# Performance work log

Measured on AMD Instinct MI355X. Metric: run time of the kernel, lower is better.

Reference implementation:

```python
import jax, jax.numpy as jnp
import numpy as np

V = 50000
D = 128
EF = 16
E = 800000
LN_EPS = 1e-5


def setup_inputs() -> dict:
    key = jax.random.key(0)
    ks = jax.random.split(key, 9)
    h = jax.random.normal(ks[0], (V, D), dtype=jnp.float32)
    edge_index = jax.random.randint(ks[1], (2, E), 0, V, dtype=jnp.int64)
    edge_attr = jax.random.normal(ks[2], (E, EF), dtype=jnp.float32)
    # msg_mlp = Linear(D+EF, D) -> ReLU -> Dropout(0) -> Linear(D, D)
    s1 = 1.0 / np.sqrt(D + EF)
    s2 = 1.0 / np.sqrt(D)
    W1 = jax.random.uniform(ks[3], (D + EF, D), minval=-s1, maxval=s1, dtype=jnp.float32)
    b1 = jax.random.uniform(ks[4], (D,), minval=-s1, maxval=s1, dtype=jnp.float32)
    W2 = jax.random.uniform(ks[5], (D, D), minval=-s2, maxval=s2, dtype=jnp.float32)
    b2 = jax.random.uniform(ks[6], (D,), minval=-s2, maxval=s2, dtype=jnp.float32)
    gamma = jnp.ones((D,), dtype=jnp.float32)
    beta = jnp.zeros((D,), dtype=jnp.float32)
    return {"h": h, "edge_index": edge_index, "edge_attr": edge_attr,
            "W1": W1, "b1": b1, "W2": W2, "b2": b2,
            "gamma": gamma, "beta": beta}


def _layer_norm(x, gamma, beta):
    mu = jnp.mean(x, axis=-1, keepdims=True)
    var = jnp.mean(jnp.square(x - mu), axis=-1, keepdims=True)
    return (x - mu) * jax.lax.rsqrt(var + LN_EPS) * gamma + beta


def reference(h, edge_index, edge_attr, W1, b1, W2, b2, gamma, beta):
    src, dst = edge_index[0], edge_index[1]
    # gather source node features, concat edge features: [E, D+EF]
    x = jnp.concatenate([h[src], edge_attr], axis=-1)
    # per-edge message MLP (dropout p=0 -> identity)
    msg = jax.nn.relu(x @ W1 + b1) @ W2 + b2  # [E, D]
    # scatter-add messages to destinations
    agg = jax.ops.segment_sum(msg, dst, num_segments=V)  # [V, D]
    # count initialized to ones BEFORE scatter_add -> denominator = 1 + in_degree
    deg = jax.ops.segment_sum(jnp.ones((E,), dtype=h.dtype), dst, num_segments=V)
    count = (1.0 + deg)[:, None]  # [V, 1]
    return _layer_norm(h + agg / count, gamma, beta)
```

## Files before the change

### kernel.cpp

```cpp
#include <hip/hip_runtime.h>
#include <hip/hip_bf16.h>

#define V 50000
#define D 128
#define EF 16
#define E_EDGES 800000
#define NT 12500
#define USTR 136
#define XESTR 40
#define CSTR 136
#define NSCAN 196
#define EGRID 1024
#define UGRID 782

typedef __attribute__((ext_vector_type(8))) __bf16 bf16x8;
typedef __attribute__((ext_vector_type(4))) float f32x4;
typedef __attribute__((ext_vector_type(2))) __fp16 fp16x2;

__device__ inline unsigned short f2bf(float f) {
    unsigned u = __float_as_uint(f);
    u += 0x7FFF + ((u >> 16) & 1);
    return (unsigned short)(u >> 16);
}
__device__ inline unsigned pack2(float a, float b) {
    return (unsigned)f2bf(a) | ((unsigned)f2bf(b) << 16);
}
__device__ inline float bf2f(unsigned short u) {
    return __uint_as_float((unsigned)u << 16);
}
__device__ inline unsigned pkbf(float a, float b) {
    union { __hip_bfloat162 h; unsigned u; } v;
    v.h = __float22bfloat162_rn(make_float2(a, b));
    return v.u;
}
__device__ inline unsigned pkf16(float a, float b) {
    union { fp16x2 h; unsigned u; } v;
    v.h = __builtin_amdgcn_cvt_pkrtz(a, b);
    return v.u;
}

__global__ __launch_bounds__(256)
void setup_kernel(const float* __restrict__ h, const int* __restrict__ ei,
                  int* __restrict__ cnt, float* __restrict__ agg,
                  const float* __restrict__ W1, const float* __restrict__ W2,
                  unsigned short* __restrict__ W1p, unsigned short* __restrict__ W2p,
                  unsigned short* __restrict__ U) {
    __shared__ __align__(16) unsigned short Hs[64 * USTR];
    const int tid = threadIdx.x;
    int idx = blockIdx.x * 256 + tid;
    *(float4*)(agg + ((size_t)idx << 2)) = (float4){0.f, 0.f, 0.f, 0.f};
    if (idx < E_EDGES) atomicAdd(&cnt[ei[E_EDGES + idx]], 1);
    if (idx < 5 * 128 * 32) {
        int kb = idx >> 12, rem = idx & 4095;
        int n = rem >> 5, kk = rem & 31;
        int k = kb * 32 + kk;
        W1p[idx] = f2bf((k < D + EF) ? W1[k * D + n] : 0.0f);
    }
    if (idx < 4 * 128 * 32) {
        int kb = idx >> 12, rem = idx & 4095;
        int n = rem >> 5, kk = rem & 31;
        W2p[idx] = f2bf(W2[(kb * 32 + kk) * D + n]);
    }
    if (blockIdx.x >= UGRID) return;

    const int lane = tid & 63;
    const int wave = tid >> 6;
    const int nlo  = lane & 15;
    const int kq   = lane >> 4;
    const int er   = tid >> 4;
    const int ec   = tid & 15;
    const int gbase = blockIdx.x << 6;

    bf16x8 B1[4][2];
    #pragma unroll
    for (int t = 0; t < 2; ++t) {
        int n = wave * 32 + t * 16 + nlo;
        #pragma unroll
        for (int kb = 0; kb < 4; ++kb) {
            union { bf16x8 v; unsigned short s[8]; } f;
            #pragma unroll
            for (int j = 0; j < 8; ++j)
                f.s[j] = f2bf(W1[(kb * 32 + (kq << 3) + j) * D + n]);
            B1[kb][t] = f.v;
        }
    }

    #pragma unroll
    for (int m = 0; m < 4; ++m) {
        int row = er + m * 16;
        int grow = gbase + row;
        unsigned* o = (unsigned*)(Hs + row * USTR + (ec << 3));
        if (grow < V) {
            const float4* p = (const float4*)(h + (size_t)grow * D + (ec << 3));
            float4 v0 = p[0], v1 = p[1];
            o[0] = pack2(v0.x, v0.y); o[1] = pack2(v0.z, v0.w);
            o[2] = pack2(v1.x, v1.y); o[3] = pack2(v1.z, v1.w);
        } else {
            o[0] = 0u; o[1] = 0u; o[2] = 0u; o[3] = 0u;
        }
    }
    __syncthreads();

    f32x4 acc[4][2];
    #pragma unroll
    for (int mt = 0; mt < 4; ++mt)
        #pragma unroll
        for (int t = 0; t < 2; ++t)
            acc[mt][t] = (f32x4){0.f, 0.f, 0.f, 0.f};

    #pragma unroll
    for (int kb = 0; kb < 4; ++kb) {
        bf16x8 A[4];
        int ko = kb * 32 + (kq << 3);
        #pragma unroll
        for (int mt = 0; mt < 4; ++mt)
            A[mt] = *(const bf16x8*)(Hs + (mt * 16 + nlo) * USTR + ko);
        #pragma unroll
        for (int mt = 0; mt < 4; ++mt)
            #pragma unroll
            for (int t = 0; t < 2; ++t)
                acc[mt][t] = __builtin_amdgcn_mfma_f32_16x16x32_bf16(A[mt], B1[kb][t], acc[mt][t], 0, 0, 0);
    }

    #pragma unroll
    for (int mt = 0; mt < 4; ++mt)
        #pragma unroll
        for (int t = 0; t < 2; ++t)
            #pragma unroll
            for (int r = 0; r < 4; ++r) {
                int row = mt * 16 + (kq << 2) + r;
                int grow = gbase + row;
                int col = wave * 32 + t * 16 + nlo;
                if (grow < V)
                    U[(size_t)grow * D + col] = f2bf(acc[mt][t][r]);
            }
}

__device__ inline int block_excl_scan(int x, int t, int* ws) {
    int lane = t & 63, w = t >> 6;
    int inc = x;
    #pragma unroll
    for (int off = 1; off < 64; off <<= 1) {
        int y = __shfl_up(inc, off);
        if (lane >= off) inc += y;
    }
    if (lane == 63) ws[w] = inc;
    __syncthreads();
    if (t == 0) {
        int r = 0;
        #pragma unroll
        for (int i = 0; i < 4; ++i) { int c = ws[i]; ws[i] = r; r += c; }
    }
    __syncthreads();
    return inc - x + ws[w];
}

__global__ __launch_bounds__(256)
void scan1_kernel(const int* __restrict__ cnt, int* __restrict__ cursor,
                  int* __restrict__ bsum) {
    __shared__ int ws[4];
    __shared__ int tot;
    int t = threadIdx.x;
    int i = blockIdx.x * 256 + t;
    int x = (i < V) ? cnt[i] : 0;
    int ex = block_excl_scan(x, t, ws);
    if (i < V) cursor[i] = ex;
    if (t == 255) tot = ex + x;
    __syncthreads();
    if (t == 0) bsum[blockIdx.x] = tot;
}

__global__ __launch_bounds__(256)
void scatter_kernel(const int* __restrict__ ei, int* __restrict__ cursor,
                    const int* __restrict__ bsum,
                    int* __restrict__ srcs, int* __restrict__ dsts,
                    int* __restrict__ eidx) {
    __shared__ int ws[4];
    __shared__ int sboff[NSCAN];
    int t = threadIdx.x;
    int x = (t < NSCAN) ? bsum[t] : 0;
    int ex = block_excl_scan(x, t, ws);
    if (t < NSCAN) sboff[t] = ex;
    __syncthreads();
    int e = blockIdx.x * 256 + t;
    int d = ei[E_EDGES + e];
    int pos = atomicAdd(&cursor[d], 1) + sboff[d >> 8];
    srcs[pos] = ei[e];
    dsts[pos] = d;
    eidx[pos] = e;
}

__global__ __launch_bounds__(256, 4)
void edge_kernel(const unsigned short* __restrict__ U,
                 const float* __restrict__ ea,
                 const int* __restrict__ srcs, const int* __restrict__ dsts,
                 const int* __restrict__ eidx,
                 const unsigned short* __restrict__ W1p, const unsigned short* __restrict__ W2p,
                 const float* __restrict__ b1, const float* __restrict__ b2,
                 float* __restrict__ agg) {
    __shared__ __align__(16) unsigned short Us[64 * USTR];
    __shared__ __align__(16) _Float16 Cs[64 * CSTR];
    __shared__ __align__(16) unsigned short Xe[64 * XESTR];
    __shared__ int sDst[2][64];

    const int tid  = threadIdx.x;
    const int lane = tid & 63;
    const int wave = tid >> 6;
    const int nlo  = lane & 15;
    const int kq   = lane >> 4;
    const int er   = tid >> 4;
    const int ec   = tid & 15;
    const int ee   = tid >> 2;
    const int eq   = tid & 3;

    bf16x8 B1e[2], B2[4][2];
    float4 b1n[2], b2n[2];
    #pragma unroll
    for (int t = 0; t < 2; ++t) {
        int n = wave * 32 + t * 16 + nlo;
        b1n[t] = *(const float4*)(b1 + wave * 32 + t * 16 + (kq << 2));
        b2n[t] = *(const float4*)(b2 + wave * 32 + t * 16 + (kq << 2));
        B1e[t] = *(const bf16x8*)(W1p + ((4 << 7) + n) * 32 + (kq << 3));
        #pragma unroll
        for (int kb = 0; kb < 4; ++kb)
            B2[kb][t] = *(const bf16x8*)(W2p + ((kb << 7) + n) * 32 + (kq << 3));
    }

    {
        unsigned* xz = (unsigned*)Xe;
        int i0 = tid, i1 = tid + 256;
        xz[(i0 >> 3) * (XESTR / 2) + 8 + (i0 & 7)] = 0u;
        xz[(i1 >> 3) * (XESTR / 2) + 8 + (i1 & 7)] = 0u;
    }

    const int base0 = blockIdx.x << 6;
    int a0 = srcs[base0 + er];
    int a1 = srcs[base0 + er + 16];
    int a2 = srcs[base0 + er + 32];
    int a3 = srcs[base0 + er + 48];
    int aev = eidx[base0 + ee];
    int ddcur = dsts[base0 + lane];
    bf16x8 pf0 = *(const bf16x8*)(U + (size_t)a0 * D + (ec << 3));
    bf16x8 pf1 = *(const bf16x8*)(U + (size_t)a1 * D + (ec << 3));
    bf16x8 pf2 = *(const bf16x8*)(U + (size_t)a2 * D + (ec << 3));
    bf16x8 pf3 = *(const bf16x8*)(U + (size_t)a3 * D + (ec << 3));
    float4 pfe = *(const float4*)(ea + (size_t)aev * EF + (eq << 2));

    int n1 = blockIdx.x + EGRID;
    int nb1 = (n1 < NT ? n1 : blockIdx.x) << 6;
    int i1s0 = srcs[nb1 + er];
    int i1s1 = srcs[nb1 + er + 16];
    int i1s2 = srcs[nb1 + er + 32];
    int i1s3 = srcs[nb1 + er + 48];
    int i1e  = eidx[nb1 + ee];
    int i1d  = dsts[nb1 + lane];

    int buf = 0;
    for (int tile = blockIdx.x; tile < NT; tile += EGRID) {
        if (tid < 64) sDst[buf][tid] = ddcur;
        *(bf16x8*)(Us + er * USTR + (ec << 3))        = pf0;
        *(bf16x8*)(Us + (er + 16) * USTR + (ec << 3)) = pf1;
        *(bf16x8*)(Us + (er + 32) * USTR + (ec << 3)) = pf2;
        *(bf16x8*)(Us + (er + 48) * USTR + (ec << 3)) = pf3;
        {
            unsigned* xp = (unsigned*)Xe + ee * (XESTR / 2) + (eq << 1);
            xp[0] = pkbf(pfe.x, pfe.y);
            xp[1] = pkbf(pfe.z, pfe.w);
        }
        __syncthreads();

        f32x4 accE[4][2];
        #pragma unroll
        for (int mt = 0; mt < 4; ++mt)
            #pragma unroll
            for (int t = 0; t < 2; ++t) {
                uint2 uu = *(const uint2*)(Us + (mt * 16 + nlo) * USTR + wave * 32 + t * 16 + (kq << 2));
                accE[mt][t][0] = bf2f((unsigned short)uu.x);
                accE[mt][t][1] = bf2f((unsigned short)(uu.x >> 16));
                accE[mt][t][2] = bf2f((unsigned short)uu.y);
                accE[mt][t][3] = bf2f((unsigned short)(uu.y >> 16));
            }
        {
            bf16x8 Xf[4];
            #pragma unroll
            for (int mt = 0; mt < 4; ++mt)
                Xf[mt] = *(const bf16x8*)(Xe + (mt * 16 + nlo) * XESTR + (kq << 3));
            #pragma unroll
            for (int mt = 0; mt < 4; ++mt)
                #pragma unroll
                for (int t = 0; t < 2; ++t)
                    accE[mt][t] = __builtin_amdgcn_mfma_f32_16x16x32_bf16(B1e[t], Xf[mt], accE[mt][t], 0, 0, 0);
        }

        #pragma unroll
        for (int mt = 0; mt < 4; ++mt)
            #pragma unroll
            for (int t = 0; t < 2; ++t) {
                uint2 yw;
                yw.x = pkbf(fmaxf(accE[mt][t][0] + b1n[t].x, 0.0f),
                            fmaxf(accE[mt][t][1] + b1n[t].y, 0.0f));
                yw.y = pkbf(fmaxf(accE[mt][t][2] + b1n[t].z, 0.0f),
                            fmaxf(accE[mt][t][3] + b1n[t].w, 0.0f));
                *(uint2*)(Us + (mt * 16 + nlo) * USTR + wave * 32 + t * 16 + (kq << 2)) = yw;
            }
        __syncthreads();

        f32x4 acc2[4][2];
        #pragma unroll
        for (int mt = 0; mt < 4; ++mt)
            #pragma unroll
            for (int t = 0; t < 2; ++t)
                acc2[mt][t] = (f32x4){0.f, 0.f, 0.f, 0.f};

        #pragma unroll
        for (int kb = 0; kb < 4; ++kb) {
            bf16x8 Yf[4];
            int ko = kb * 32 + (kq << 3);
            #pragma unroll
            for (int mt = 0; mt < 4; ++mt)
                Yf[mt] = *(const bf16x8*)(Us + (mt * 16 + nlo) * USTR + ko);
            #pragma unroll
            for (int mt = 0; mt < 4; ++mt)
                #pragma unroll
                for (int t = 0; t < 2; ++t)
                    acc2[mt][t] = __builtin_amdgcn_mfma_f32_16x16x32_bf16(B2[kb][t], Yf[mt], acc2[mt][t], 0, 0, 0);
        }

        #pragma unroll
        for (int mt = 0; mt < 4; ++mt)
            #pragma unroll
            for (int t = 0; t < 2; ++t) {
                uint2 cw;
                cw.x = pkf16(acc2[mt][t][0] + b2n[t].x, acc2[mt][t][1] + b2n[t].y);
                cw.y = pkf16(acc2[mt][t][2] + b2n[t].z, acc2[mt][t][3] + b2n[t].w);
                *(uint2*)((unsigned short*)Cs + (size_t)(mt * 16 + nlo) * CSTR + wave * 32 + t * 16 + (kq << 2)) = cw;
            }
        __syncthreads();

        int n2 = tile + 2 * EGRID;
        int nb2 = (n2 < NT ? n2 : tile) << 6;
        int i2s0 = srcs[nb2 + er];
        int i2s1 = srcs[nb2 + er + 16];
        int i2s2 = srcs[nb2 + er + 32];
        int i2s3 = srcs[nb2 + er + 48];
        int i2e  = eidx[nb2 + ee];
        int i2d  = dsts[nb2 + lane];

        bf16x8 q0 = *(const bf16x8*)(U + (size_t)i1s0 * D + (ec << 3));
        bf16x8 q1 = *(const bf16x8*)(U + (size_t)i1s1 * D + (ec << 3));
        bf16x8 q2 = *(const bf16x8*)(U + (size_t)i1s2 * D + (ec << 3));
        bf16x8 q3 = *(const bf16x8*)(U + (size_t)i1s3 * D + (ec << 3));
        float4 qe = *(const float4*)(ea + (size_t)i1e * EF + (eq << 2));
        int nextdd = i1d;

        {
            int col = tid & 127;
            int rbase = (tid >> 7) << 5;
            float sum = 0.f;
            int cur = sDst[buf][rbase];
            for (int i = 0; i < 32; ++i) {
                int d = sDst[buf][rbase + i];
                if (d != cur) {
                    atomicAdd(&agg[(size_t)cur * D + col], sum);
                    sum = 0.f;
                    cur = d;
                }
                sum += (float)Cs[(rbase + i) * CSTR + col];
            }
            atomicAdd(&agg[(size_t)cur * D + col], sum);
        }

        pf0 = q0; pf1 = q1; pf2 = q2; pf3 = q3; pfe = qe; ddcur = nextdd;
        i1s0 = i2s0; i1s1 = i2s1; i1s2 = i2s2; i1s3 = i2s3; i1e = i2e; i1d = i2d;
        buf ^= 1;
    }
}

__global__ __launch_bounds__(256)
void finalize_kernel(const float* __restrict__ h, const float* __restrict__ agg,
                     const int* __restrict__ cnt,
                     const float* __restrict__ gamma, const float* __restrict__ beta,
                     float* __restrict__ out) {
    int wave = threadIdx.x >> 6, lane = threadIdx.x & 63;
    int v = blockIdx.x * 4 + wave;
    if (v >= V) return;
    float inv = 1.0f / (1.0f + (float)cnt[v]);
    const float* hr = h + (size_t)v * D;
    const float* ar = agg + (size_t)v * D;
    float x0 = hr[lane]      + ar[lane]      * inv;
    float x1 = hr[lane + 64] + ar[lane + 64] * inv;
    float s = x0 + x1;
    #pragma unroll
    for (int m = 32; m; m >>= 1) s += __shfl_xor(s, m);
    float mu = s * (1.0f / 128.0f);
    float d0 = x0 - mu, d1 = x1 - mu;
    float vs = d0 * d0 + d1 * d1;
    #pragma unroll
    for (int m = 32; m; m >>= 1) vs += __shfl_xor(vs, m);
    float rs = rsqrtf(vs * (1.0f / 128.0f) + 1e-5f);
    out[(size_t)v * D + lane]      = d0 * rs * gamma[lane]      + beta[lane];
    out[(size_t)v * D + 64 + lane] = d1 * rs * gamma[lane + 64] + beta[lane + 64];
}

extern "C" void kernel_launch(void* const* d_in, const int* in_sizes, int n_in,
                              void* d_out, int out_size, void* d_ws, size_t ws_size,
                              hipStream_t stream) {
    const float* h     = (const float*)d_in[0];
    const int*   ei    = (const int*)d_in[1];
    const float* ea    = (const float*)d_in[2];
    const float* W1    = (const float*)d_in[3];
    const float* b1    = (const float*)d_in[4];
    const float* W2    = (const float*)d_in[5];
    const float* b2    = (const float*)d_in[6];
    const float* gamma = (const float*)d_in[7];
    const float* beta  = (const float*)d_in[8];
    float* out = (float*)d_out;

    char* ws = (char*)d_ws;
    float*          agg    = (float*)ws;
    int*            cnt    = (int*)(ws + 25600000);
    int*            cursor = (int*)(ws + 25800000);
    int*            bsum   = (int*)(ws + 26000000);
    int*            srcs   = (int*)(ws + 26000800);
    int*            dsts   = (int*)(ws + 29200800);
    int*            eidx   = (int*)(ws + 32400800);
    unsigned short* W1p    = (unsigned short*)(ws + 35600800);
    unsigned short* W2p    = (unsigned short*)(ws + 35641760);
    unsigned short* U      = (unsigned short*)(ws + 35674528);

    (void)hipMemsetAsync(cnt, 0, 200000, stream);
    setup_kernel<<<6250, 256, 0, stream>>>(h, ei, cnt, agg, W1, W2, W1p, W2p, U);
    scan1_kernel<<<NSCAN, 256, 0, stream>>>(cnt, cursor, bsum);
    scatter_kernel<<<3125, 256, 0, stream>>>(ei, cursor, bsum, srcs, dsts, eidx);
    edge_kernel<<<EGRID, 256, 0, stream>>>(U, ea, srcs, dsts, eidx, W1p, W2p, b1, b2, agg);
    finalize_kernel<<<12500, 256, 0, stream>>>(h, agg, cnt, gamma, beta, out);
}
```

Measured before the change: 302.5 us.

## Double edge tile to 128 rows with shared Us/Cs LDS union

Grows the per-block edge tile from 64 to 128 edges, so each wave reuses its register-resident W1/W2 fragments across twice as many MFMA rows and the segmented scatter runs over longer sorted runs, which means fewer atomics. The Us and Cs LDS buffers are overlaid in a union to hold shared memory down. This adds extra barriers, removes the double-buffered sDst, and lowers the occupancy hint from 4 to 3 blocks per CU with a grid of 768. Register pressure rises from 8 prefetched gather vectors and 16 accumulators, which risks spills or lower occupancy.

```diff
diff --git a/kernel.cpp b/kernel.cpp
--- a/kernel.cpp
+++ b/kernel.cpp
@@ -5,12 +5,11 @@
 #define D 128
 #define EF 16
 #define E_EDGES 800000
-#define NT 12500
+#define NIT 6250
 #define USTR 136
 #define XESTR 40
-#define CSTR 136
 #define NSCAN 196
-#define EGRID 1024
+#define EGRID 768
 #define UGRID 782
 
 typedef __attribute__((ext_vector_type(8))) __bf16 bf16x8;
@@ -190,7 +189,7 @@
     eidx[pos] = e;
 }
 
-__global__ __launch_bounds__(256, 4)
+__global__ __launch_bounds__(256, 3)
 void edge_kernel(const unsigned short* __restrict__ U,
                  const float* __restrict__ ea,
                  const int* __restrict__ srcs, const int* __restrict__ dsts,
@@ -198,10 +197,13 @@
                  const unsigned short* __restrict__ W1p, const unsigned short* __restrict__ W2p,
                  const float* __restrict__ b1, const float* __restrict__ b2,
                  float* __restrict__ agg) {
-    __shared__ __align__(16) unsigned short Us[64 * USTR];
-    __shared__ __align__(16) _Float16 Cs[64 * CSTR];
-    __shared__ __align__(16) unsigned short Xe[64 * XESTR];
-    __shared__ int sDst[2][64];
+    union SU {
+        unsigned short Us[128 * USTR];
+        _Float16 Cs[128 * USTR];
+    };
+    __shared__ __align__(16) SU u;
+    __shared__ __align__(16) unsigned short Xe[128 * XESTR];
+    __shared__ int sDst[128];
 
     const int tid  = threadIdx.x;
     const int lane = tid & 63;
@@ -210,8 +212,8 @@
     const int kq   = lane >> 4;
     const int er   = tid >> 4;
     const int ec   = tid & 15;
-    const int ee   = tid >> 2;
-    const int eq   = tid & 3;
+    const int ee2  = tid >> 1;
+    const int eq2  = tid & 1;
 
     bf16x8 B1e[2], B2[4][2];
     float4 b1n[2], b2n[2];
@@ -226,153 +228,156 @@
             B2[kb][t] = *(const bf16x8*)(W2p + ((kb << 7) + n) * 32 + (kq << 3));
     }
 
+    #pragma unroll
+    for (int j = 0; j < 4; ++j) {
+        int idx = (tid << 2) + j;
+        ((unsigned*)Xe)[(idx >> 3) * (XESTR / 2) + 8 + (idx & 7)] = 0u;
+    }
+
+    const int base0 = blockIdx.x << 7;
+    int dd = (tid < 128) ? dsts[base0 + tid] : 0;
+    bf16x8 pf[8];
     {
-        unsigned* xz = (unsigned*)Xe;
-        int i0 = tid, i1 = tid + 256;
-        xz[(i0 >> 3) * (XESTR / 2) + 8 + (i0 & 7)] = 0u;
-        xz[(i1 >> 3) * (XESTR / 2) + 8 + (i1 & 7)] = 0u;
-    }
-
-    const int base0 = blockIdx.x << 6;
-    int a0 = srcs[base0 + er];
-    int a1 = srcs[base0 + er + 16];
-    int a2 = srcs[base0 + er + 32];
-    int a3 = srcs[base0 + er + 48];
-    int aev = eidx[base0 + ee];
-    int ddcur = dsts[base0 + lane];
-    bf16x8 pf0 = *(const bf16x8*)(U + (size_t)a0 * D + (ec << 3));
-    bf16x8 pf1 = *(const bf16x8*)(U + (size_t)a1 * D + (ec << 3));
-    bf16x8 pf2 = *(const bf16x8*)(U + (size_t)a2 * D + (ec << 3));
-    bf16x8 pf3 = *(const bf16x8*)(U + (size_t)a3 * D + (ec << 3));
-    float4 pfe = *(const float4*)(ea + (size_t)aev * EF + (eq << 2));
+        int s[8];
+        #pragma unroll
+        for (int k = 0; k < 8; ++k) s[k] = srcs[base0 + er + (k << 4)];
+        #pragma unroll
+        for (int k = 0; k < 8; ++k)
+            pf[k] = *(const bf16x8*)(U + (size_t)s[k] * D + (ec << 3));
+    }
+    int ae0 = eidx[base0 + ee2];
+    float4 pe0 = *(const float4*)(ea + (size_t)ae0 * EF + (eq2 << 3));
+    float4 pe1 = *(const float4*)(ea + (size_t)ae0 * EF + (eq2 << 3) + 4);
 
     int n1 = blockIdx.x + EGRID;
-    int nb1 = (n1 < NT ? n1 : blockIdx.x) << 6;
-    int i1s0 = srcs[nb1 + er];
-    int i1s1 = srcs[nb1 + er + 16];
-    int i1s2 = srcs[nb1 + er + 32];
-    int i1s3 = srcs[nb1 + er + 48];
-    int i1e  = eidx[nb1 + ee];
-    int i1d  = dsts[nb1 + lane];
-
-    int buf = 0;
-    for (int tile = blockIdx.x; tile < NT; tile += EGRID) {
-        if (tid < 64) sDst[buf][tid] = ddcur;
-        *(bf16x8*)(Us + er * USTR + (ec << 3))        = pf0;
-        *(bf16x8*)(Us + (er + 16) * USTR + (ec << 3)) = pf1;
-        *(bf16x8*)(Us + (er + 32) * USTR + (ec << 3)) = pf2;
-        *(bf16x8*)(Us + (er + 48) * USTR + (ec << 3)) = pf3;
+    int nb1 = (n1 < NIT ? n1 : blockIdx.x) << 7;
+    int j1s[8];
+    #pragma unroll
+    for (int k = 0; k < 8; ++k) j1s[k] = srcs[nb1 + er + (k << 4)];
+    int j1e = eidx[nb1 + ee2];
+    int j1d = (tid < 128) ? dsts[nb1 + tid] : 0;
+
+    for (int it = blockIdx.x; it < NIT; it += EGRID) {
+        if (tid < 128) sDst[tid] = dd;
+        #pragma unroll
+        for (int k = 0; k < 8; ++k)
+            *(bf16x8*)(u.Us + (er + (k << 4)) * USTR + (ec << 3)) = pf[k];
         {
-            unsigned* xp = (unsigned*)Xe + ee * (XESTR / 2) + (eq << 1);
-            xp[0] = pkbf(pfe.x, pfe.y);
-            xp[1] = pkbf(pfe.z, pfe.w);
+            unsigned* xp = (unsigned*)Xe + ee2 * (XESTR / 2) + (eq2 << 2);
+            xp[0] = pkbf(pe0.x, pe0.y);
+            xp[1] = pkbf(pe0.z, pe0.w);
+            xp[2] = pkbf(pe1.x, pe1.y);
+            xp[3] = pkbf(pe1.z, pe1.w);
         }
         __syncthreads();
 
-        f32x4 accE[4][2];
-        #pragma unroll
-        for (int mt = 0; mt < 4; ++mt)
-            #pragma unroll
-            for (int t = 0; t < 2; ++t) {
-                uint2 uu = *(const uint2*)(Us + (mt * 16 + nlo) * USTR + wave * 32 + t * 16 + (kq << 2));
-                accE[mt][t][0] = bf2f((unsigned short)uu.x);
-                accE[mt][t][1] = bf2f((unsigned short)(uu.x >> 16));
-                accE[mt][t][2] = bf2f((unsigned short)uu.y);
-                accE[mt][t][3] = bf2f((unsigned short)(uu.y >> 16));
-            }
-        {
+        #pragma unroll
+        for (int mtb = 0; mtb < 8; mtb += 4) {
+            f32x4 accE[4][2];
+            #pragma unroll
+            for (int i = 0; i < 4; ++i)
+                #pragma unroll
+                for (int t = 0; t < 2; ++t) {
+                    uint2 uu = *(const uint2*)(u.Us + ((mtb + i) * 16 + nlo) * USTR + wave * 32 + t * 16 + (kq << 2));
+                    accE[i][t][0] = bf2f((unsigned short)uu.x);
+                    accE[i][t][1] = bf2f((unsigned short)(uu.x >> 16));
+                    accE[i][t][2] = bf2f((unsigned short)uu.y);
+                    accE[i][t][3] = bf2f((unsigned short)(uu.y >> 16));
+                }
             bf16x8 Xf[4];
             #pragma unroll
-            for (int mt = 0; mt < 4; ++mt)
-                Xf[mt] = *(const bf16x8*)(Xe + (mt * 16 + nlo) * XESTR + (kq << 3));
-            #pragma unroll
-            for (int mt = 0; mt < 4; ++mt)
+            for (int i = 0; i < 4; ++i)
+                Xf[i] = *(const bf16x8*)(Xe + ((mtb + i) * 16 + nlo) * XESTR + (kq << 3));
+            #pragma unroll
+            for (int i = 0; i < 4; ++i)
                 #pragma unroll
                 for (int t = 0; t < 2; ++t)
-                    accE[mt][t] = __builtin_amdgcn_mfma_f32_16x16x32_bf16(B1e[t], Xf[mt], accE[mt][t], 0, 0, 0);
-        }
-
-        #pragma unroll
-        for (int mt = 0; mt < 4; ++mt)
-            #pragma unroll
-            for (int t = 0; t < 2; ++t) {
-                uint2 yw;
-                yw.x = pkbf(fmaxf(accE[mt][t][0] + b1n[t].x, 0.0f),
-                            fmaxf(accE[mt][t][1] + b1n[t].y, 0.0f));
-                yw.y = pkbf(fmaxf(accE[mt][t][2] + b1n[t].z, 0.0f),
-                            fmaxf(accE[mt][t][3] + b1n[t].w, 0.0f));
-                *(uint2*)(Us + (mt * 16 + nlo) * USTR + wave * 32 + t * 16 + (kq << 2)) = yw;
-            }
+                    accE[i][t] = __builtin_amdgcn_mfma_f32_16x16x32_bf16(B1e[t], Xf[i], accE[i][t], 0, 0, 0);
+            #pragma unroll
+            for (int i = 0; i < 4; ++i)
+                #pragma unroll
+                for (int t = 0; t < 2; ++t) {
+                    uint2 yw;
+                    yw.x = pkbf(fmaxf(accE[i][t][0] + b1n[t].x, 0.0f),
+                                fmaxf(accE[i][t][1] + b1n[t].y, 0.0f));
+                    yw.y = pkbf(fmaxf(accE[i][t][2] + b1n[t].z, 0.0f),
+                                fmaxf(accE[i][t][3] + b1n[t].w, 0.0f));
+                    *(uint2*)(u.Us + ((mtb + i) * 16 + nlo) * USTR + wave * 32 + t * 16 + (kq << 2)) = yw;
+                }
+        }
         __syncthreads();
 
-        f32x4 acc2[4][2];
-        #pragma unroll
-        for (int mt = 0; mt < 4; ++mt)
+        int n2 = it + 2 * EGRID;
+        int nb2 = (n2 < NIT ? n2 : it) << 7;
+        int j2s[8];
+        #pragma unroll
+        for (int k = 0; k < 8; ++k) j2s[k] = srcs[nb2 + er + (k << 4)];
+        int j2e = eidx[nb2 + ee2];
+        int j2d = (tid < 128) ? dsts[nb2 + tid] : 0;
+
+        f32x4 acc2[8][2];
+        #pragma unroll
+        for (int mt = 0; mt < 8; ++mt)
             #pragma unroll
             for (int t = 0; t < 2; ++t)
                 acc2[mt][t] = (f32x4){0.f, 0.f, 0.f, 0.f};
 
         #pragma unroll
         for (int kb = 0; kb < 4; ++kb) {
-            bf16x8 Yf[4];
+            bf16x8 Yf[8];
             int ko = kb * 32 + (kq << 3);
             #pragma unroll
-            for (int mt = 0; mt < 4; ++mt)
-                Yf[mt] = *(const bf16x8*)(Us + (mt * 16 + nlo) * USTR + ko);
-            #pragma unroll
-            for (int mt = 0; mt < 4; ++mt)
+            for (int mt = 0; mt < 8; ++mt)
+                Yf[mt] = *(const bf16x8*)(u.Us + (mt * 16 + nlo) * USTR + ko);
+            #pragma unroll
+            for (int mt = 0; mt < 8; ++mt)
                 #pragma unroll
                 for (int t = 0; t < 2; ++t)
                     acc2[mt][t] = __builtin_amdgcn_mfma_f32_16x16x32_bf16(B2[kb][t], Yf[mt], acc2[mt][t], 0, 0, 0);
         }
-
-        #pragma unroll
-        for (int mt = 0; mt < 4; ++mt)
+        __syncthreads();
+
+        #pragma unroll
+        for (int mt = 0; mt < 8; ++mt)
             #pragma unroll
             for (int t = 0; t < 2; ++t) {
                 uint2 cw;
                 cw.x = pkf16(acc2[mt][t][0] + b2n[t].x, acc2[mt][t][1] + b2n[t].y);
                 cw.y = pkf16(acc2[mt][t][2] + b2n[t].z, acc2[mt][t][3] + b2n[t].w);
-                *(uint2*)((unsigned short*)Cs + (size_t)(mt * 16 + nlo) * CSTR + wave * 32 + t * 16 + (kq << 2)) = cw;
+                *(uint2*)((unsigned short*)u.Cs + (size_t)(mt * 16 + nlo) * USTR + wave * 32 + t * 16 + (kq << 2)) = cw;
             }
         __syncthreads();
 
-        int n2 = tile + 2 * EGRID;
-        int nb2 = (n2 < NT ? n2 : tile) << 6;
-        int i2s0 = srcs[nb2 + er];
-        int i2s1 = srcs[nb2 + er + 16];
-        int i2s2 = srcs[nb2 + er + 32];
-        int i2s3 = srcs[nb2 + er + 48];
-        int i2e  = eidx[nb2 + ee];
-        int i2d  = dsts[nb2 + lane];
-
-        bf16x8 q0 = *(const bf16x8*)(U + (size_t)i1s0 * D + (ec << 3));
-        bf16x8 q1 = *(const bf16x8*)(U + (size_t)i1s1 * D + (ec << 3));
-        bf16x8 q2 = *(const bf16x8*)(U + (size_t)i1s2 * D + (ec << 3));
-        bf16x8 q3 = *(const bf16x8*)(U + (size_t)i1s3 * D + (ec << 3));
-        float4 qe = *(const float4*)(ea + (size_t)i1e * EF + (eq << 2));
-        int nextdd = i1d;
+        bf16x8 qf[8];
+        #pragma unroll
+        for (int k = 0; k < 8; ++k)
+            qf[k] = *(const bf16x8*)(U + (size_t)j1s[k] * D + (ec << 3));
+        float4 qe0 = *(const float4*)(ea + (size_t)j1e * EF + (eq2 << 3));
+        float4 qe1 = *(const float4*)(ea + (size_t)j1e * EF + (eq2 << 3) + 4);
+        int nd = j1d;
 
         {
             int col = tid & 127;
-            int rbase = (tid >> 7) << 5;
+            int rbase = (tid >> 7) << 6;
             float sum = 0.f;
-            int cur = sDst[buf][rbase];
-            for (int i = 0; i < 32; ++i) {
-                int d = sDst[buf][rbase + i];
+            int cur = sDst[rbase];
+            for (int i = 0; i < 64; ++i) {
+                int d = sDst[rbase + i];
                 if (d != cur) {
                     atomicAdd(&agg[(size_t)cur * D + col], sum);
                     sum = 0.f;
                     cur = d;
                 }
-                sum += (float)Cs[(rbase + i) * CSTR + col];
+                sum += (float)u.Cs[(rbase + i) * USTR + col];
             }
             atomicAdd(&agg[(size_t)cur * D + col], sum);
         }
-
-        pf0 = q0; pf1 = q1; pf2 = q2; pf3 = q3; pfe = qe; ddcur = nextdd;
-        i1s0 = i2s0; i1s1 = i2s1; i1s2 = i2s2; i1s3 = i2s3; i1e = i2e; i1d = i2d;
-        buf ^= 1;
+        __syncthreads();
+
+        #pragma unroll
+        for (int k = 0; k < 8; ++k) { pf[k] = qf[k]; j1s[k] = j2s[k]; }
+        pe0 = qe0; pe1 = qe1; dd = nd;
+        j1e = j2e; j1d = j2d;
     }
 }
 
```

New measurement: 415.9 us. 1.37x slower.
